# Performance work log

Hardware: AMD Instinct MI355X
Metric: run time of the kernel (lower is better)

Reference implementation:

```python
import jax, jax.numpy as jnp
import numpy as np

B = 4096          # batch of vectors
D = 768           # embedding_size
P = 96            # partition (number of sub-quantizers)
C = 256           # centroids per partition
SD = D // P       # sub-vector dim = 8


def setup_inputs() -> dict:
    key = jax.random.key(0)
    k1, k2 = jax.random.split(key)
    vecs = jax.random.normal(k1, (B, D), dtype=jnp.float32)
    # nn.Parameter(torch.empty(P, C, SD).uniform_(-0.1, 0.1))
    codebook = jax.random.uniform(k2, (P, C, SD), dtype=jnp.float32,
                                  minval=-0.1, maxval=0.1)
    return {"vecs": vecs, "codebook": codebook}


def _quantize(vecs, codebook):
    # vecs: [B, D] -> [B, P, SD]
    v = vecs.reshape(vecs.shape[0], P, SD)
    # proba = -sum((v - c)^2) expanded to avoid the [B,P,C,SD] intermediate:
    # ||v||^2 - 2 v.c + ||c||^2  per (b, p, c)
    v_sq = jnp.sum(v * v, axis=-1, keepdims=True)            # [B, P, 1]
    c_sq = jnp.sum(codebook * codebook, axis=-1)             # [P, C]
    vc = jnp.einsum('bpd,pcd->bpc', v, codebook)             # [B, P, C]
    proba = -(v_sq - 2.0 * vc + c_sq[None])                  # [B, P, C]
    assign = jax.nn.softmax(proba, axis=-1)                  # [B, P, C]
    # straight-through estimator: hard one-hot fwd, soft grad
    index = jnp.argmax(assign, axis=-1)                      # [B, P]
    assign_hard = jax.nn.one_hot(index, C, dtype=assign.dtype)
    assign_ste = jax.lax.stop_gradient(assign_hard - assign) + assign
    # reconstruction: [B,P,C] @ [P,C,SD] -> [B,P,SD] -> [B,D]
    q = jnp.einsum('bpc,pcd->bpd', assign_ste, codebook)
    return q.reshape(vecs.shape[0], -1)


def reference(vecs, codebook):
    return _quantize(vecs, codebook)
```

## Files before the change

kernel.cpp:

```cpp
#include <hip/hip_runtime.h>
#include <cmath>

constexpr int B  = 4096;
constexpr int D  = 768;
constexpr int P  = 96;
constexpr int C  = 256;
constexpr int SD = 8;

constexpr int TPB  = 256;
constexpr int WPB  = 4;
constexpr int CPW  = C / WPB;
constexpr int ROWS = 4;

__device__ __forceinline__ float tree8(float q0, float q1, float q2, float q3,
                                       float q4, float q5, float q6, float q7)
{
#pragma clang fp contract(off)
    return ((q0 + q1) + (q2 + q3)) + ((q4 + q5) + (q6 + q7));
}

__device__ __forceinline__ float proba_np(const float* __restrict__ cbf,
                                          const float* __restrict__ csq,
                                          int c, float4 va, float4 vb, float vsq)
{
#pragma clang fp contract(off)
    float4 ca = ((const float4*)cbf)[2 * c];
    float4 cb = ((const float4*)cbf)[2 * c + 1];
    float p0 = va.x * ca.x, p1 = va.y * ca.y, p2 = va.z * ca.z, p3 = va.w * ca.w;
    float p4 = vb.x * cb.x, p5 = vb.y * cb.y, p6 = vb.z * cb.z, p7 = vb.w * cb.w;
    float l0 = p0 + p4, l1 = p1 + p5, l2 = p2 + p6, l3 = p3 + p7;
    float vc = (l0 + l2) + (l1 + l3);
    float tt = vsq - 2.0f * vc;
    float u  = tt + csq[c];
    return -u;
}

__device__ __attribute__((noinline))
int exact_search(const float* __restrict__ cbf, const float* __restrict__ csq,
                 float4 va, float4 vb, float vsq)
{
#pragma clang fp contract(off)
    float best = -3.402823466e38f, second = -3.402823466e38f;
    int bi = 0;
    for (int c = 0; c < C; ++c) {
        float pr = proba_np(cbf, csq, c, va, vb, vsq);
        if (pr > best)        { second = best; best = pr; bi = c; }
        else if (pr > second) { second = pr; }
    }
    int idx = bi;

    if (best - second <= 1.0e-6f) {
        float m = best;
        float r0[8] = {0,0,0,0,0,0,0,0};
        float r1[8] = {0,0,0,0,0,0,0,0};
        for (int cg = 0; cg < 16; ++cg) {
            #pragma unroll
            for (int j = 0; j < 8; ++j) {
                float pr = proba_np(cbf, csq, cg * 8 + j, va, vb, vsq);
                r0[j] += expf(pr - m);
            }
        }
        for (int cg = 16; cg < 32; ++cg) {
            #pragma unroll
            for (int j = 0; j < 8; ++j) {
                float pr = proba_np(cbf, csq, cg * 8 + j, va, vb, vsq);
                r1[j] += expf(pr - m);
            }
        }
        float sum = tree8(r0[0],r0[1],r0[2],r0[3],r0[4],r0[5],r0[6],r0[7])
                  + tree8(r1[0],r1[1],r1[2],r1[3],r1[4],r1[5],r1[6],r1[7]);
        float abest = -1.0f;
        int   ai    = 0;
        for (int c = 0; c < C; ++c) {
            float pr = proba_np(cbf, csq, c, va, vb, vsq);
            float e  = expf(pr - m);
            float a  = e / sum;
            if (a > abest) { abest = a; ai = c; }
        }
        idx = ai;
    }
    return idx;
}

__global__ __launch_bounds__(TPB, 6)
void pq_split_kernel(const float* __restrict__ vecs,
                     const float* __restrict__ codebook,
                     float* __restrict__ out)
{
    __shared__ float  cbf [C * SD];
    __shared__ float  csqn[C];
    __shared__ float  csqh[C];
    __shared__ float2 part_bs[WPB][ROWS][64];
    __shared__ int    part_i [WPB][ROWS][64];

    const int p = blockIdx.x;
    const int t = threadIdx.x;
    const int w = t >> 6;
    const int l = t & 63;
    const int rowbase = blockIdx.y * (64 * ROWS);

    const float4* src = (const float4*)(codebook + (size_t)p * C * SD);
    ((float4*)cbf)[t]       = src[t];
    ((float4*)cbf)[t + 256] = src[t + 256];
    __syncthreads();

    {
        const float* cc = cbf + t * SD;
        float q0 = cc[0]*cc[0], q1 = cc[1]*cc[1], q2 = cc[2]*cc[2], q3 = cc[3]*cc[3];
        float q4 = cc[4]*cc[4], q5 = cc[5]*cc[5], q6 = cc[6]*cc[6], q7 = cc[7]*cc[7];
        float s = tree8(q0,q1,q2,q3,q4,q5,q6,q7);
        csqn[t] = s;
        csqh[t] = -0.5f * s;
    }
    __syncthreads();

    float4 va[ROWS], vb[ROWS];
    #pragma unroll
    for (int r = 0; r < ROWS; ++r) {
        const float* vptr = vecs + (size_t)(rowbase + 64 * r + l) * D + (size_t)p * SD;
        va[r] = ((const float4*)vptr)[0];
        vb[r] = ((const float4*)vptr)[1];
    }

    float best[ROWS], second[ROWS];
    int   bi[ROWS];
    #pragma unroll
    for (int r = 0; r < ROWS; ++r) {
        best[r] = -3.402823466e38f; second[r] = -3.402823466e38f; bi[r] = 0;
    }

    const int c0 = w * CPW;
    #pragma unroll 2
    for (int ci = 0; ci < CPW; ++ci) {
        const int c = c0 + ci;
        float4 ca = ((const float4*)cbf)[2 * c];
        float4 cb = ((const float4*)cbf)[2 * c + 1];
        float  ch = csqh[c];
        #pragma unroll
        for (int r = 0; r < ROWS; ++r) {
            float s = fmaf(va[r].x, ca.x, ch);
            s = fmaf(va[r].y, ca.y, s);
            s = fmaf(va[r].z, ca.z, s);
            s = fmaf(va[r].w, ca.w, s);
            s = fmaf(vb[r].x, cb.x, s);
            s = fmaf(vb[r].y, cb.y, s);
            s = fmaf(vb[r].z, cb.z, s);
            s = fmaf(vb[r].w, cb.w, s);
            bool gt = s > best[r];
            second[r] = fmaxf(second[r], fminf(s, best[r]));
            bi[r]     = gt ? c : bi[r];
            best[r]   = fmaxf(s, best[r]);
        }
    }

    #pragma unroll
    for (int r = 0; r < ROWS; ++r) {
        part_bs[w][r][l] = make_float2(best[r], second[r]);
        part_i [w][r][l] = bi[r];
    }
    __syncthreads();

    {
        float Bst = -3.402823466e38f, Snd = -3.402823466e38f;
        int   I   = 0;
        #pragma unroll
        for (int ww = 0; ww < WPB; ++ww) {
            float2 bs = part_bs[ww][w][l];
            int    iw = part_i [ww][w][l];
            bool gt = bs.x > Bst;
            Snd = fmaxf(Snd, fminf(bs.x, Bst));
            Snd = fmaxf(Snd, bs.y);
            I   = gt ? iw : I;
            Bst = fmaxf(Bst, bs.x);
        }

        const int row = rowbase + t;
        int idx = I;
        if (Bst - Snd <= 2.0e-5f) {
            const float* vptr = vecs + (size_t)row * D + (size_t)p * SD;
            float4 xa = ((const float4*)vptr)[0];
            float4 xb = ((const float4*)vptr)[1];
            float q0 = xa.x*xa.x, q1 = xa.y*xa.y, q2 = xa.z*xa.z, q3 = xa.w*xa.w;
            float q4 = xb.x*xb.x, q5 = xb.y*xb.y, q6 = xb.z*xb.z, q7 = xb.w*xb.w;
            float vsq = tree8(q0,q1,q2,q3,q4,q5,q6,q7);
            idx = exact_search(cbf, csqn, xa, xb, vsq);
        }

        float4 o0 = ((const float4*)cbf)[2 * idx];
        float4 o1 = ((const float4*)cbf)[2 * idx + 1];
        float4* op = (float4*)(out + (size_t)row * D + (size_t)p * SD);
        op[0] = o0;
        op[1] = o1;
    }
}

extern "C" void kernel_launch(void* const* d_in, const int* in_sizes, int n_in,
                              void* d_out, int out_size, void* d_ws, size_t ws_size,
                              hipStream_t stream)
{
    const float* vecs     = (const float*)d_in[0];
    const float* codebook = (const float*)d_in[1];
    float*       out      = (float*)d_out;

    dim3 grid(P, B / (64 * ROWS));
    dim3 block(TPB);
    pq_split_kernel<<<grid, block, 0, stream>>>(vecs, codebook, out);
}
```

Before: 173.0 us.

## Halve rows per block to double grid size and unroll centroid loop by four

Cuts the rows each thread handles from 4 to 2, so each block covers 128 rows and the grid doubles to 96x32 blocks. The centroid loop is unrolled by 4 and batches LDS loads, including a float4 load of four csq values. Only the first 128 threads do the cross-wave merge and write output. The goal is more blocks and wave parallelism, at the price of loading and squaring the codebook in twice as many blocks and leaving half the threads idle in the final phase.

```diff
diff --git a/kernel.cpp b/kernel.cpp
--- a/kernel.cpp
+++ b/kernel.cpp
@@ -8,9 +8,8 @@
 constexpr int SD = 8;
 
 constexpr int TPB  = 256;
-constexpr int WPB  = 4;
-constexpr int CPW  = C / WPB;
-constexpr int ROWS = 4;
+constexpr int ROWS = 2;
+constexpr int CPW  = C / 4;
 
 __device__ __forceinline__ float tree8(float q0, float q1, float q2, float q3,
                                        float q4, float q5, float q6, float q7)
@@ -83,21 +82,21 @@
 }
 
 __global__ __launch_bounds__(TPB, 6)
-void pq_split_kernel(const float* __restrict__ vecs,
-                     const float* __restrict__ codebook,
-                     float* __restrict__ out)
+void pq_occ_kernel(const float* __restrict__ vecs,
+                   const float* __restrict__ codebook,
+                   float* __restrict__ out)
 {
     __shared__ float  cbf [C * SD];
     __shared__ float  csqn[C];
     __shared__ float  csqh[C];
-    __shared__ float2 part_bs[WPB][ROWS][64];
-    __shared__ int    part_i [WPB][ROWS][64];
+    __shared__ float2 part_bs[4][128];
+    __shared__ int    part_i [4][128];
 
     const int p = blockIdx.x;
     const int t = threadIdx.x;
     const int w = t >> 6;
     const int l = t & 63;
-    const int rowbase = blockIdx.y * (64 * ROWS);
+    const int rowbase = blockIdx.y * 128;
 
     const float4* src = (const float4*)(codebook + (size_t)p * C * SD);
     ((float4*)cbf)[t]       = src[t];
@@ -130,47 +129,53 @@
     }
 
     const int c0 = w * CPW;
-    #pragma unroll 2
-    for (int ci = 0; ci < CPW; ++ci) {
-        const int c = c0 + ci;
-        float4 ca = ((const float4*)cbf)[2 * c];
-        float4 cb = ((const float4*)cbf)[2 * c + 1];
-        float  ch = csqh[c];
+    for (int c = c0; c < c0 + CPW; c += 4) {
+        float4 A[4], Bv[4];
         #pragma unroll
-        for (int r = 0; r < ROWS; ++r) {
-            float s = fmaf(va[r].x, ca.x, ch);
-            s = fmaf(va[r].y, ca.y, s);
-            s = fmaf(va[r].z, ca.z, s);
-            s = fmaf(va[r].w, ca.w, s);
-            s = fmaf(vb[r].x, cb.x, s);
-            s = fmaf(vb[r].y, cb.y, s);
-            s = fmaf(vb[r].z, cb.z, s);
-            s = fmaf(vb[r].w, cb.w, s);
-            bool gt = s > best[r];
-            second[r] = fmaxf(second[r], fminf(s, best[r]));
-            bi[r]     = gt ? c : bi[r];
-            best[r]   = fmaxf(s, best[r]);
+        for (int u = 0; u < 4; ++u) {
+            A[u]  = ((const float4*)cbf)[2 * (c + u)];
+            Bv[u] = ((const float4*)cbf)[2 * (c + u) + 1];
+        }
+        float4 H4 = *(const float4*)(csqh + c);
+        float  H[4] = { H4.x, H4.y, H4.z, H4.w };
+        #pragma unroll
+        for (int u = 0; u < 4; ++u) {
+            #pragma unroll
+            for (int r = 0; r < ROWS; ++r) {
+                float s = fmaf(va[r].x, A[u].x, H[u]);
+                s = fmaf(va[r].y, A[u].y, s);
+                s = fmaf(va[r].z, A[u].z, s);
+                s = fmaf(va[r].w, A[u].w, s);
+                s = fmaf(vb[r].x, Bv[u].x, s);
+                s = fmaf(vb[r].y, Bv[u].y, s);
+                s = fmaf(vb[r].z, Bv[u].z, s);
+                s = fmaf(vb[r].w, Bv[u].w, s);
+                bool gt = s > best[r];
+                second[r] = fmaxf(second[r], fminf(s, best[r]));
+                bi[r]     = gt ? (c + u) : bi[r];
+                best[r]   = fmaxf(s, best[r]);
+            }
         }
     }
 
     #pragma unroll
     for (int r = 0; r < ROWS; ++r) {
-        part_bs[w][r][l] = make_float2(best[r], second[r]);
-        part_i [w][r][l] = bi[r];
+        part_bs[w][64 * r + l] = make_float2(best[r], second[r]);
+        part_i [w][64 * r + l] = bi[r];
     }
     __syncthreads();
 
-    {
+    if (t < 128) {
         float Bst = -3.402823466e38f, Snd = -3.402823466e38f;
         int   I   = 0;
         #pragma unroll
-        for (int ww = 0; ww < WPB; ++ww) {
-            float2 bs = part_bs[ww][w][l];
-            int    iw = part_i [ww][w][l];
+        for (int q = 0; q < 4; ++q) {
+            float2 bs = part_bs[q][t];
+            int    iq = part_i [q][t];
             bool gt = bs.x > Bst;
             Snd = fmaxf(Snd, fminf(bs.x, Bst));
             Snd = fmaxf(Snd, bs.y);
-            I   = gt ? iw : I;
+            I   = gt ? iq : I;
             Bst = fmaxf(Bst, bs.x);
         }
 
@@ -202,7 +207,7 @@
     const float* codebook = (const float*)d_in[1];
     float*       out      = (float*)d_out;
 
-    dim3 grid(P, B / (64 * ROWS));
+    dim3 grid(P, B / 128);
     dim3 block(TPB);
-    pq_split_kernel<<<grid, block, 0, stream>>>(vecs, codebook, out);
-}
+    pq_occ_kernel<<<grid, block, 0, stream>>>(vecs, codebook, out);
+}
```

Measured after the change: 178.0 us. 1.03x slower.

## Compute codebook scores with split-bf16 MFMA and wave-level shuffle argmax

Applied to the files above, without the earlier changes.

Replaces the scalar FMA distance loop with a 16x16x32 bf16 MFMA. Each fp32 vector and codeword is split into high and low bf16 parts packed along K, so one instruction accumulates hi*hi+hi*lo+lo*hi products and keeps near-fp32 accuracy. Each wave now handles 16 rows against all 256 centroids and reduces best/second with xor shuffles, so the shared-memory cross-wave reduction and its barrier are gone. The near-tie threshold is widened so the exact fp32 fallback catches precision differences, which may send more rows down the slow path. Grid size grows, and the final write uses only a quarter of the lanes.

```diff
diff --git a/kernel.cpp b/kernel.cpp
--- a/kernel.cpp
+++ b/kernel.cpp
@@ -7,10 +7,17 @@
 constexpr int C  = 256;
 constexpr int SD = 8;
 
-constexpr int TPB  = 256;
-constexpr int WPB  = 4;
-constexpr int CPW  = C / WPB;
-constexpr int ROWS = 4;
+typedef __attribute__((ext_vector_type(8))) short  short8;
+typedef __attribute__((ext_vector_type(4))) float  floatx4;
+
+__device__ __forceinline__ unsigned short f2bf(float f) {
+    unsigned u = __float_as_uint(f);
+    u += 0x7FFFu + ((u >> 16) & 1u);
+    return (unsigned short)(u >> 16);
+}
+__device__ __forceinline__ float bf2f(unsigned short s) {
+    return __uint_as_float(((unsigned)s) << 16);
+}
 
 __device__ __forceinline__ float tree8(float q0, float q1, float q2, float q3,
                                        float q4, float q5, float q6, float q7)
@@ -82,22 +89,24 @@
     return idx;
 }
 
-__global__ __launch_bounds__(TPB, 6)
-void pq_split_kernel(const float* __restrict__ vecs,
-                     const float* __restrict__ codebook,
-                     float* __restrict__ out)
+__global__ __launch_bounds__(256, 4)
+void pq_mfma_kernel(const float* __restrict__ vecs,
+                    const float* __restrict__ codebook,
+                    float* __restrict__ out)
 {
     __shared__ float  cbf [C * SD];
     __shared__ float  csqn[C];
     __shared__ float  csqh[C];
-    __shared__ float2 part_bs[WPB][ROWS][64];
-    __shared__ int    part_i [WPB][ROWS][64];
+    __shared__ short8 cbh [C];
+    __shared__ short8 cbl [C];
 
     const int p = blockIdx.x;
     const int t = threadIdx.x;
     const int w = t >> 6;
     const int l = t & 63;
-    const int rowbase = blockIdx.y * (64 * ROWS);
+    const int n = l & 15;
+    const int q = l >> 4;
+    const int rowbase = (blockIdx.y * 4 + w) * 16;
 
     const float4* src = (const float4*)(codebook + (size_t)p * C * SD);
     ((float4*)cbf)[t]       = src[t];
@@ -111,83 +120,84 @@
         float s = tree8(q0,q1,q2,q3,q4,q5,q6,q7);
         csqn[t] = s;
         csqh[t] = -0.5f * s;
+        unsigned short* hh = (unsigned short*)&cbh[t];
+        unsigned short* ll = (unsigned short*)&cbl[t];
+        #pragma unroll
+        for (int j = 0; j < SD; ++j) {
+            unsigned short hi = f2bf(cc[j]);
+            hh[j] = hi;
+            ll[j] = f2bf(cc[j] - bf2f(hi));
+        }
     }
     __syncthreads();
 
-    float4 va[ROWS], vb[ROWS];
-    #pragma unroll
-    for (int r = 0; r < ROWS; ++r) {
-        const float* vptr = vecs + (size_t)(rowbase + 64 * r + l) * D + (size_t)p * SD;
-        va[r] = ((const float4*)vptr)[0];
-        vb[r] = ((const float4*)vptr)[1];
-    }
-
-    float best[ROWS], second[ROWS];
-    int   bi[ROWS];
-    #pragma unroll
-    for (int r = 0; r < ROWS; ++r) {
-        best[r] = -3.402823466e38f; second[r] = -3.402823466e38f; bi[r] = 0;
-    }
-
-    const int c0 = w * CPW;
-    #pragma unroll 2
-    for (int ci = 0; ci < CPW; ++ci) {
-        const int c = c0 + ci;
-        float4 ca = ((const float4*)cbf)[2 * c];
-        float4 cb = ((const float4*)cbf)[2 * c + 1];
-        float  ch = csqh[c];
-        #pragma unroll
-        for (int r = 0; r < ROWS; ++r) {
-            float s = fmaf(va[r].x, ca.x, ch);
-            s = fmaf(va[r].y, ca.y, s);
-            s = fmaf(va[r].z, ca.z, s);
-            s = fmaf(va[r].w, ca.w, s);
-            s = fmaf(vb[r].x, cb.x, s);
-            s = fmaf(vb[r].y, cb.y, s);
-            s = fmaf(vb[r].z, cb.z, s);
-            s = fmaf(vb[r].w, cb.w, s);
+    short8 afrag;
+    {
+        const float* vp = vecs + (size_t)(rowbase + n) * D + (size_t)p * SD;
+        float4 v0 = ((const float4*)vp)[0];
+        float4 v1 = ((const float4*)vp)[1];
+        float vf[8] = { v0.x, v0.y, v0.z, v0.w, v1.x, v1.y, v1.z, v1.w };
+        const bool hiA = ((q & 1) == 0);
+        #pragma unroll
+        for (int j = 0; j < SD; ++j) {
+            unsigned short hi = f2bf(vf[j]);
+            unsigned short lo = f2bf(vf[j] - bf2f(hi));
+            ((unsigned short*)&afrag)[j] = (short)(hiA ? hi : lo);
+        }
+    }
+    const short8* Bsrc = (q == 0 || q == 3) ? cbh : cbl;
+
+    float best[4]   = { -3.402823466e38f, -3.402823466e38f,
+                        -3.402823466e38f, -3.402823466e38f };
+    float second[4] = { -3.402823466e38f, -3.402823466e38f,
+                        -3.402823466e38f, -3.402823466e38f };
+    int   idx[4]    = { 0, 0, 0, 0 };
+
+    for (int tt = 0; tt < 16; ++tt) {
+        const int c = tt * 16 + n;
+        float h = csqh[c];
+        floatx4 acc = { h, h, h, h };
+        short8 bfrag = Bsrc[c];
+        acc = __builtin_amdgcn_mfma_f32_16x16x32_bf16(afrag, bfrag, acc, 0, 0, 0);
+        #pragma unroll
+        for (int r = 0; r < 4; ++r) {
+            float s = acc[r];
             bool gt = s > best[r];
             second[r] = fmaxf(second[r], fminf(s, best[r]));
-            bi[r]     = gt ? c : bi[r];
+            idx[r]    = gt ? c : idx[r];
             best[r]   = fmaxf(s, best[r]);
         }
     }
 
     #pragma unroll
-    for (int r = 0; r < ROWS; ++r) {
-        part_bs[w][r][l] = make_float2(best[r], second[r]);
-        part_i [w][r][l] = bi[r];
-    }
-    __syncthreads();
-
-    {
-        float Bst = -3.402823466e38f, Snd = -3.402823466e38f;
-        int   I   = 0;
-        #pragma unroll
-        for (int ww = 0; ww < WPB; ++ww) {
-            float2 bs = part_bs[ww][w][l];
-            int    iw = part_i [ww][w][l];
-            bool gt = bs.x > Bst;
-            Snd = fmaxf(Snd, fminf(bs.x, Bst));
-            Snd = fmaxf(Snd, bs.y);
-            I   = gt ? iw : I;
-            Bst = fmaxf(Bst, bs.x);
-        }
-
-        const int row = rowbase + t;
-        int idx = I;
-        if (Bst - Snd <= 2.0e-5f) {
-            const float* vptr = vecs + (size_t)row * D + (size_t)p * SD;
-            float4 xa = ((const float4*)vptr)[0];
-            float4 xb = ((const float4*)vptr)[1];
+    for (int m = 1; m < 16; m <<= 1) {
+        #pragma unroll
+        for (int r = 0; r < 4; ++r) {
+            float ob = __shfl_xor(best[r],   m, 64);
+            float os = __shfl_xor(second[r], m, 64);
+            int   oi = __shfl_xor(idx[r],    m, 64);
+            bool better = (ob > best[r]) || (ob == best[r] && oi < idx[r]);
+            second[r] = fmaxf(fmaxf(second[r], os), fminf(ob, best[r]));
+            idx[r]    = better ? oi : idx[r];
+            best[r]   = fmaxf(best[r], ob);
+        }
+    }
+
+    if (n < 4) {
+        const int r   = n;
+        const int row = rowbase + q * 4 + n;
+        int id = idx[r];
+        if (best[r] - second[r] <= 2.0e-4f) {
+            const float* vp = vecs + (size_t)row * D + (size_t)p * SD;
+            float4 xa = ((const float4*)vp)[0];
+            float4 xb = ((const float4*)vp)[1];
             float q0 = xa.x*xa.x, q1 = xa.y*xa.y, q2 = xa.z*xa.z, q3 = xa.w*xa.w;
             float q4 = xb.x*xb.x, q5 = xb.y*xb.y, q6 = xb.z*xb.z, q7 = xb.w*xb.w;
             float vsq = tree8(q0,q1,q2,q3,q4,q5,q6,q7);
-            idx = exact_search(cbf, csqn, xa, xb, vsq);
-        }
-
-        float4 o0 = ((const float4*)cbf)[2 * idx];
-        float4 o1 = ((const float4*)cbf)[2 * idx + 1];
+            id = exact_search(cbf, csqn, xa, xb, vsq);
+        }
+        float4 o0 = ((const float4*)cbf)[2 * id];
+        float4 o1 = ((const float4*)cbf)[2 * id + 1];
         float4* op = (float4*)(out + (size_t)row * D + (size_t)p * SD);
         op[0] = o0;
         op[1] = o1;
@@ -202,7 +212,7 @@
     const float* codebook = (const float*)d_in[1];
     float*       out      = (float*)d_out;
 
-    dim3 grid(P, B / (64 * ROWS));
-    dim3 block(TPB);
-    pq_split_kernel<<<grid, block, 0, stream>>>(vecs, codebook, out);
-}
+    dim3 grid(P, B / 64);
+    dim3 block(256);
+    pq_mfma_kernel<<<grid, block, 0, stream>>>(vecs, codebook, out);
+}
```

Result: slower. 197.4 us (+14.1%).
